# Kernel optimization log

Hardware: AMD Instinct MI355X
Metric: run time of the kernel (lower is better)

The kernel has to match this reference:

```python
import jax, jax.numpy as jnp
import numpy as np
from jax import lax

B, T, E, H = 32, 512, 256, 512

def setup_inputs() -> dict:
    key = jax.random.key(0)
    ks = jax.random.split(key, 7)
    s = 1.0 / np.sqrt(H)  # PyTorch RNN init range
    u = lambda k, sh: jax.random.uniform(k, sh, jnp.float32, -s, s)
    return {
        "xs": jax.random.normal(ks[0], (B, T, E), jnp.float32),
        "w_ih0": u(ks[1], (2, H, E)),      # [dir, H, in]
        "w_hh0": u(ks[2], (2, H, H)),
        "b0":    u(ks[3], (2, 2, H)),      # [dir, (b_ih,b_hh), H]
        "w_ih1": u(ks[4], (2, H, 2 * H)),
        "w_hh1": u(ks[5], (2, H, H)),
        "b1":    u(ks[6], (2, 2, H)),
    }

def _rnn_dir(x_tbi, w_ih, w_hh, b_ih, b_hh, reverse):
    # Precompute the input GEMM for all timesteps: [T,B,H]
    pre = jnp.einsum('tbi,hi->tbh', x_tbi, w_ih) + b_ih + b_hh
    h0 = jnp.zeros((x_tbi.shape[1], w_hh.shape[0]), x_tbi.dtype)
    def step(h, p):
        h = jnp.tanh(p + h @ w_hh.T)
        return h, h
    _, hs = lax.scan(step, h0, pre, reverse=reverse)  # ys aligned with xs order
    hy = hs[0] if reverse else hs[-1]
    return hs, hy

def _layer(x_tbi, w_ih, w_hh, b):
    hf, hyf = _rnn_dir(x_tbi, w_ih[0], w_hh[0], b[0, 0], b[0, 1], False)
    hb, hyb = _rnn_dir(x_tbi, w_ih[1], w_hh[1], b[1, 0], b[1, 1], True)
    return jnp.concatenate([hf, hb], axis=-1), jnp.stack([hyf, hyb])

def reference(xs, w_ih0, w_hh0, b0, w_ih1, w_hh1, b1):
    x = jnp.transpose(xs, (1, 0, 2))          # batch_first -> [T,B,E]
    h1, hy0 = _layer(x, w_ih0, w_hh0, b0)     # [T,B,2H], [2,B,H]
    h2, hy1 = _layer(h1, w_ih1, w_hh1, b1)
    hs = jnp.transpose(h2, (1, 0, 2))         # [B,T,2H]
    hy = jnp.concatenate([hy0, hy1], axis=0)  # [4,B,H] layer-major like PyTorch
    # F.dropout with p=0.0 is identity
    return (hs, hy)
```

## Files before the change

kernel.cpp:

```cpp
#include <hip/hip_runtime.h>
#include <hip/hip_fp16.h>


#define T_ 512
#define B_ 32
#define E_ 256
#define H_ 512

using half8 = _Float16 __attribute__((ext_vector_type(8)));
using f32x4 = float __attribute__((ext_vector_type(4)));
typedef unsigned long long u64;
typedef unsigned int u32;

static constexpr size_t OFF_PRE   = 0;
static constexpr size_t OFF_XH1   = 32ull << 20;
static constexpr size_t OFF_X0H   = 64ull << 20;
static constexpr size_t OFF_W0H   = 72ull << 20;
static constexpr size_t OFF_W1H   = OFF_W0H + (512ull << 10);
static constexpr size_t OFF_WHH   = OFF_W1H + (2ull << 20);
static constexpr size_t OFF_BS    = OFF_WHH + (2ull << 20);
static constexpr size_t OFF_HX    = OFF_BS + (8ull << 10);
static constexpr size_t OFF_FLG   = OFF_HX + (512ull << 10);
static constexpr size_t OFF_CTL   = OFF_FLG + 512;
static constexpr size_t ZERO_SIZE = (512ull << 10) + 1024;

static constexpr size_t HX_LAYER_STRIDE = 2 * 2 * 32 * 256;
static constexpr size_t HX_DIR_STRIDE   = 2 * 32 * 256;

__device__ __forceinline__ float fast_tanh(float x) {
    float cx = fminf(fmaxf(x, -9.0f), 9.0f);
    float e2 = __expf(2.0f * cx);
    return (e2 - 1.0f) * __builtin_amdgcn_rcpf(e2 + 1.0f);
}

__global__ void prep_kernel(const float* __restrict__ xs,
                            const float* __restrict__ wih0,
                            const float* __restrict__ whh0,
                            const float* __restrict__ b0,
                            const float* __restrict__ wih1,
                            const float* __restrict__ whh1,
                            const float* __restrict__ b1,
                            _Float16* __restrict__ x0h,
                            _Float16* __restrict__ w0h,
                            _Float16* __restrict__ w1h,
                            _Float16* __restrict__ whh,
                            float* __restrict__ bsum)
{
    const int N0 = T_ * B_ * E_;
    const int N1 = 2 * H_ * E_;
    const int N2 = 2 * H_ * 2*H_;
    const int N3 = 2 * H_ * H_;
    const int total = N0 + N1 + N2 + 2 * N3 + 2048;
    for (int idx = blockIdx.x * blockDim.x + threadIdx.x; idx < total;
         idx += gridDim.x * blockDim.x) {
        int i = idx;
        if (i < N0) {
            int t = i >> 13;
            int r = i & 8191;
            int b = r >> 8;
            int e = r & 255;
            x0h[i] = (_Float16)xs[((size_t)(b << 9) + t) * 256 + e];
        } else if ((i -= N0) < N1) {
            w0h[i] = (_Float16)wih0[i];
        } else if ((i -= N1) < N2) {
            w1h[i] = (_Float16)wih1[i];
        } else if ((i -= N2) < N3) {
            whh[i] = (_Float16)whh0[i];
        } else if ((i -= N3) < N3) {
            whh[N3 + i] = (_Float16)whh1[i];
        } else {
            i -= N3;
            int layer = i >> 10;
            int r = i & 1023;
            int d = r >> 9;
            int j = r & 511;
            const float* bb = layer ? b1 : b0;
            bsum[i] = bb[d * 1024 + j] + bb[d * 1024 + 512 + j];
        }
    }
}

__global__ __launch_bounds__(256, 2)
void gemm_kernel(const _Float16* __restrict__ X,
                 const _Float16* __restrict__ W,
                 const float* __restrict__ bias,
                 _Float16* __restrict__ out, int K)
{
    __shared__ _Float16 Ash[64][72];
    __shared__ _Float16 Bsh[64][72];
    const int m0 = blockIdx.x * 64, n0 = blockIdx.y * 64, d = blockIdx.z;
    const _Float16* Wd = W + (size_t)d * 512 * K;
    const int tid = threadIdx.x;
    const int l = tid & 63, w = tid >> 6;
    const int wm = w & 1, wn = w >> 1;
    const int lm = l & 15, q = l >> 4;
    f32x4 c[2][2] = {};
    for (int kk = 0; kk < K; kk += 64) {
        for (int ci = tid; ci < 512; ci += 256) {
            int row = ci >> 3, col = (ci & 7) * 8;
            *(half8*)&Ash[row][col] =
                *(const half8*)&X[(size_t)(m0 + row) * K + kk + col];
            *(half8*)&Bsh[row][col] =
                *(const half8*)&Wd[(size_t)(n0 + row) * K + kk + col];
        }
        __syncthreads();
        for (int kt = 0; kt < 2; ++kt) {
            const int kof = kt * 32 + q * 8;
            half8 a0 = *(const half8*)&Ash[wm * 32 + lm][kof];
            half8 a1 = *(const half8*)&Ash[wm * 32 + 16 + lm][kof];
            half8 b0f = *(const half8*)&Bsh[wn * 32 + lm][kof];
            half8 b1f = *(const half8*)&Bsh[wn * 32 + 16 + lm][kof];
            c[0][0] = __builtin_amdgcn_mfma_f32_16x16x32_f16(a0, b0f, c[0][0], 0, 0, 0);
            c[0][1] = __builtin_amdgcn_mfma_f32_16x16x32_f16(a0, b1f, c[0][1], 0, 0, 0);
            c[1][0] = __builtin_amdgcn_mfma_f32_16x16x32_f16(a1, b0f, c[1][0], 0, 0, 0);
            c[1][1] = __builtin_amdgcn_mfma_f32_16x16x32_f16(a1, b1f, c[1][1], 0, 0, 0);
        }
        __syncthreads();
    }
    _Float16* outd = out + (size_t)d * 16384 * 512;
    for (int mi = 0; mi < 2; ++mi)
        for (int ni = 0; ni < 2; ++ni) {
            int col = n0 + wn * 32 + ni * 16 + lm;
            float bv = bias[d * 512 + col];
            for (int r = 0; r < 4; ++r) {
                int rowm = m0 + wm * 32 + mi * 16 + q * 4 + r;
                outd[(size_t)rowm * 512 + col] = (_Float16)(c[mi][ni][r] + bv);
            }
        }
}

__global__ __launch_bounds__(256)
void rnn_kernel(const _Float16* __restrict__ pre,
                const _Float16* __restrict__ whh,
                u64* __restrict__ hx,
                u32* __restrict__ flgL,
                u32* __restrict__ ctl,
                _Float16* __restrict__ xh1,
                float* __restrict__ dout,
                int layer)
{
    __shared__ uint4 As[2][64 * 33];
    __shared__ int sh_role, sh_slot;

    const int tid = threadIdx.x;

    if (tid == 0) {
        int xcc;
        asm volatile("s_getreg_b32 %0, hwreg(HW_REG_XCC_ID)" : "=s"(xcc));
        xcc &= 7;
        u32 slot = __hip_atomic_fetch_add(&ctl[xcc], 1u, __ATOMIC_RELAXED,
                                          __HIP_MEMORY_SCOPE_SYSTEM);
        int role = 0;
        if (slot < 16u) {
            if (slot == 15u) {
                u32 r = __hip_atomic_fetch_add(&ctl[8], 1u, __ATOMIC_ACQ_REL,
                                               __HIP_MEMORY_SCOPE_SYSTEM);
                role = (r < 2u) ? (int)r + 1 : 3;
                __hip_atomic_store(&ctl[16 + xcc], (u32)role, __ATOMIC_RELEASE,
                                   __HIP_MEMORY_SCOPE_SYSTEM);
            } else {
                long it = 0;
                while (true) {
                    u32 r = __hip_atomic_load(&ctl[16 + xcc], __ATOMIC_ACQUIRE,
                                              __HIP_MEMORY_SCOPE_SYSTEM);
                    if (r) { role = (int)r; break; }
                    if (++it > 10000000) { role = 3; break; }
                }
            }
        }
        sh_role = role;
        sh_slot = (int)slot;
    }
    __syncthreads();
    const int role = sh_role;
    const int g = sh_slot;
    if (role == 0 || role == 3) return;
    const int d = role - 1;

    const int wv = tid >> 6, l = tid & 63;
    const int lm = l & 15, q = l >> 4;
    const int wm = wv & 1, wn = wv >> 1;
    const int jn = g * 32 + wn * 16;
    const int bA = wm * 16 + lm;
    const int bq = wm * 16 + q * 4;

    half8 Bf[16];
    {
        const _Float16* wrow = whh + ((size_t)d * 512 + jn + lm) * 512;
#pragma unroll
        for (int kt = 0; kt < 16; ++kt)
            Bf[kt] = *(const half8*)&wrow[kt * 32 + q * 8];
    }

    u64* hbd = hx + (size_t)d * HX_DIR_STRIDE;
    u32* flg = flgL + d * 32;
    const int jp_pub = (jn + (lm & ~1)) >> 1;
    const int scat_base = ((tid >> 2) * 33) * 4 + (tid & 3);

    for (int s = 0; s < T_; ++s) {
        const int t = d ? (T_ - 1 - s) : s;

        const _Float16* prow = pre + ((size_t)d * 16384 + (size_t)t * B_) * 512 + jn + lm;
        _Float16 pv[4];
#pragma unroll
        for (int r = 0; r < 4; ++r)
            pv[r] = prow[(size_t)(bq + r) * 512];

        {
            const u32 need = (u32)s;
            bool ok;
            do {
                u32 f = (l < 16)
                    ? __hip_atomic_load(&flg[l], __ATOMIC_RELAXED,
                                        __HIP_MEMORY_SCOPE_AGENT)
                    : 0xFFFFFFFFu;
                ok = __all(f >= need);
            } while (!ok);
        }

        const u64* src = hbd + (size_t)(s & 1) * 8192 + tid;
        const unsigned tag = (unsigned)s;
        u64 wvv[32];
        bool stale = true;
        do {
#pragma unroll
            for (int i = 0; i < 32; ++i)
                wvv[i] = __hip_atomic_load(&src[i * 256],
                                           __ATOMIC_RELAXED, __HIP_MEMORY_SCOPE_AGENT);
            bool ok = true;
#pragma unroll
            for (int i = 0; i < 32; ++i)
                ok &= ((unsigned)(wvv[i] >> 32) == tag);
            stale = __any(!ok);
        } while (stale);

        u32* AsW = (u32*)&As[s & 1][0];
#pragma unroll
        for (int i = 0; i < 32; ++i)
            AsW[scat_base + i * 4] = (u32)wvv[i];
        __syncthreads();

        f32x4 c0, c1;
#pragma unroll
        for (int r = 0; r < 4; ++r) { c0[r] = (float)pv[r]; c1[r] = 0.0f; }
#pragma unroll
        for (int kt = 0; kt < 16; ++kt) {
            union { uint4 u; half8 h; } cv;
            cv.u = As[s & 1][(kt * 4 + q) * 33 + bA];
            if (kt & 1) c1 = __builtin_amdgcn_mfma_f32_16x16x32_f16(cv.h, Bf[kt], c1, 0, 0, 0);
            else        c0 = __builtin_amdgcn_mfma_f32_16x16x32_f16(cv.h, Bf[kt], c0, 0, 0, 0);
        }

        u64* dst = hbd + (size_t)((s + 1) & 1) * 8192;
        const u64 tagw = ((u64)(unsigned)(s + 1)) << 32;
        const int j = jn + lm;
        float hv[4];
        unsigned hb[4];
#pragma unroll
        for (int r = 0; r < 4; ++r) {
            hv[r] = fast_tanh(c0[r] + c1[r]);
            union { _Float16 f; unsigned short u; } cb;
            cb.f = (_Float16)hv[r];
            hb[r] = cb.u;
        }
#pragma unroll
        for (int r = 0; r < 4; ++r) {
            unsigned p = __shfl_xor(hb[r], 1, 64);
            unsigned lo = (l & 1) ? p : hb[r];
            unsigned hi = (l & 1) ? hb[r] : p;
            if ((r >> 1) == (l & 1)) {
                u64 word = tagw | ((u64)hi << 16) | lo;
                __hip_atomic_store(&dst[(size_t)(bq + r) * 256 + jp_pub], word,
                                   __ATOMIC_RELAXED, __HIP_MEMORY_SCOPE_AGENT);
            }
        }
        __syncthreads();
        if (tid == 0)
            __hip_atomic_store(&flg[g], (u32)(s + 1), __ATOMIC_RELAXED,
                               __HIP_MEMORY_SCOPE_AGENT);

#pragma unroll
        for (int r = 0; r < 4; ++r) {
            const int b = bq + r;
            if (layer == 0) {
                xh1[((size_t)t * B_ + b) * 1024 + d * 512 + j] = (_Float16)hv[r];
            } else {
                dout[((size_t)b * T_ + t) * 1024 + d * 512 + j] = hv[r];
            }
            if (s == T_ - 1) {
                dout[16777216ull + ((size_t)(layer * 2 + d) * B_ + b) * 512 + j] = hv[r];
            }
        }
    }
}

extern "C" void kernel_launch(void* const* d_in, const int* in_sizes, int n_in,
                              void* d_out, int out_size, void* d_ws, size_t ws_size,
                              hipStream_t stream)
{
    const float* xs   = (const float*)d_in[0];
    const float* wih0 = (const float*)d_in[1];
    const float* whh0 = (const float*)d_in[2];
    const float* b0   = (const float*)d_in[3];
    const float* wih1 = (const float*)d_in[4];
    const float* whh1 = (const float*)d_in[5];
    const float* b1   = (const float*)d_in[6];

    char* ws = (char*)d_ws;
    _Float16* pre  = (_Float16*)(ws + OFF_PRE);
    _Float16* xh1  = (_Float16*)(ws + OFF_XH1);
    _Float16* x0h  = (_Float16*)(ws + OFF_X0H);
    _Float16* w0h  = (_Float16*)(ws + OFF_W0H);
    _Float16* w1h  = (_Float16*)(ws + OFF_W1H);
    _Float16* whh  = (_Float16*)(ws + OFF_WHH);
    float*    bsum = (float*)(ws + OFF_BS);
    u64*      hx   = (u64*)(ws + OFF_HX);
    u32*      flg  = (u32*)(ws + OFF_FLG);
    u32*      ctl  = (u32*)(ws + OFF_CTL);
    float*    out  = (float*)d_out;

    (void)hipMemsetAsync(ws + OFF_HX, 0, ZERO_SIZE, stream);

    prep_kernel<<<2048, 256, 0, stream>>>(xs, wih0, whh0, b0, wih1, whh1, b1,
                                          x0h, w0h, w1h, whh, bsum);

    gemm_kernel<<<dim3(256, 8, 2), 256, 0, stream>>>(x0h, w0h, bsum, pre, 256);
    rnn_kernel<<<256, 256, 0, stream>>>(pre, whh, hx, flg, ctl, xh1, out, 0);

    gemm_kernel<<<dim3(256, 8, 2), 256, 0, stream>>>(xh1, w1h, bsum + 1024, pre, 1024);
    rnn_kernel<<<256, 256, 0, stream>>>(pre, whh + 2 * 512 * 512,
                                        hx + HX_LAYER_STRIDE, flg + 64, ctl + 32,
                                        xh1, out, 1);
}
```

Measured before the change: 3.133 ms.

## Drop flag polling, batch hidden-state stores via LDS, spin idle blocks

```diff
diff --git a/kernel.cpp b/kernel.cpp
--- a/kernel.cpp
+++ b/kernel.cpp
@@ -20,8 +20,7 @@
 static constexpr size_t OFF_WHH   = OFF_W1H + (2ull << 20);
 static constexpr size_t OFF_BS    = OFF_WHH + (2ull << 20);
 static constexpr size_t OFF_HX    = OFF_BS + (8ull << 10);
-static constexpr size_t OFF_FLG   = OFF_HX + (512ull << 10);
-static constexpr size_t OFF_CTL   = OFF_FLG + 512;
+static constexpr size_t OFF_CTL   = OFF_HX + (512ull << 10);
 static constexpr size_t ZERO_SIZE = (512ull << 10) + 1024;
 
 static constexpr size_t HX_LAYER_STRIDE = 2 * 2 * 32 * 256;
@@ -31,6 +30,12 @@
     float cx = fminf(fmaxf(x, -9.0f), 9.0f);
     float e2 = __expf(2.0f * cx);
     return (e2 - 1.0f) * __builtin_amdgcn_rcpf(e2 + 1.0f);
+}
+
+__device__ __forceinline__ void lds_barrier() {
+    __builtin_amdgcn_sched_barrier(0);
+    asm volatile("s_waitcnt lgkmcnt(0)\n\ts_barrier" ::: "memory");
+    __builtin_amdgcn_sched_barrier(0);
 }
 
 __global__ void prep_kernel(const float* __restrict__ xs,
@@ -133,13 +138,13 @@
 void rnn_kernel(const _Float16* __restrict__ pre,
                 const _Float16* __restrict__ whh,
                 u64* __restrict__ hx,
-                u32* __restrict__ flgL,
                 u32* __restrict__ ctl,
                 _Float16* __restrict__ xh1,
                 float* __restrict__ dout,
                 int layer)
 {
     __shared__ uint4 As[2][64 * 33];
+    __shared__ float stF[8 * 32 * 36];
     __shared__ int sh_role, sh_slot;
 
     const int tid = threadIdx.x;
@@ -164,7 +169,7 @@
                     u32 r = __hip_atomic_load(&ctl[16 + xcc], __ATOMIC_ACQUIRE,
                                               __HIP_MEMORY_SCOPE_SYSTEM);
                     if (r) { role = (int)r; break; }
-                    if (++it > 10000000) { role = 3; break; }
+                    if (++it > 100000000) { role = 3; break; }
                 }
             }
         }
@@ -174,7 +179,23 @@
     __syncthreads();
     const int role = sh_role;
     const int g = sh_slot;
-    if (role == 0 || role == 3) return;
+    if (role == 0 || role == 3) {
+        float ha = 1.0f + (float)(tid & 31) * 1e-7f;
+        float hc = 1.0f - (float)(tid & 7) * 1e-7f;
+        for (int it = 0; it < 60000; ++it) {
+#pragma unroll 32
+            for (int u = 0; u < 32; ++u) {
+                ha = __builtin_fmaf(ha, 0.99999988f, 1e-9f);
+                hc = __builtin_fmaf(hc, 1.00000012f, -1e-9f);
+            }
+            if ((it & 15) == 0) {
+                if (__hip_atomic_load(&ctl[24], __ATOMIC_RELAXED,
+                                      __HIP_MEMORY_SCOPE_SYSTEM)) break;
+            }
+        }
+        asm volatile("" :: "v"(ha), "v"(hc));
+        return;
+    }
     const int d = role - 1;
 
     const int wv = tid >> 6, l = tid & 63;
@@ -183,6 +204,7 @@
     const int jn = g * 32 + wn * 16;
     const int bA = wm * 16 + lm;
     const int bq = wm * 16 + q * 4;
+    const int jl = wn * 16 + lm;
 
     half8 Bf[16];
     {
@@ -193,7 +215,6 @@
     }
 
     u64* hbd = hx + (size_t)d * HX_DIR_STRIDE;
-    u32* flg = flgL + d * 32;
     const int jp_pub = (jn + (lm & ~1)) >> 1;
     const int scat_base = ((tid >> 2) * 33) * 4 + (tid & 3);
 
@@ -205,40 +226,31 @@
 #pragma unroll
         for (int r = 0; r < 4; ++r)
             pv[r] = prow[(size_t)(bq + r) * 512];
-
-        {
-            const u32 need = (u32)s;
-            bool ok;
-            do {
-                u32 f = (l < 16)
-                    ? __hip_atomic_load(&flg[l], __ATOMIC_RELAXED,
-                                        __HIP_MEMORY_SCOPE_AGENT)
-                    : 0xFFFFFFFFu;
-                ok = __all(f >= need);
-            } while (!ok);
-        }
 
         const u64* src = hbd + (size_t)(s & 1) * 8192 + tid;
         const unsigned tag = (unsigned)s;
         u64 wvv[32];
-        bool stale = true;
-        do {
-#pragma unroll
-            for (int i = 0; i < 32; ++i)
-                wvv[i] = __hip_atomic_load(&src[i * 256],
-                                           __ATOMIC_RELAXED, __HIP_MEMORY_SCOPE_AGENT);
-            bool ok = true;
-#pragma unroll
-            for (int i = 0; i < 32; ++i)
-                ok &= ((unsigned)(wvv[i] >> 32) == tag);
-            stale = __any(!ok);
-        } while (stale);
+        {
+            bool stale = true;
+            long it = 0;
+            do {
+#pragma unroll
+                for (int i = 0; i < 32; ++i)
+                    wvv[i] = __hip_atomic_load(&src[i * 256],
+                                               __ATOMIC_RELAXED, __HIP_MEMORY_SCOPE_AGENT);
+                bool ok = true;
+#pragma unroll
+                for (int i = 0; i < 32; ++i)
+                    ok &= ((unsigned)(wvv[i] >> 32) == tag);
+                stale = __any(!ok);
+            } while (stale && ++it < 2000000);
+        }
 
         u32* AsW = (u32*)&As[s & 1][0];
 #pragma unroll
         for (int i = 0; i < 32; ++i)
             AsW[scat_base + i * 4] = (u32)wvv[i];
-        __syncthreads();
+        lds_barrier();
 
         f32x4 c0, c1;
 #pragma unroll
@@ -274,24 +286,43 @@
                                    __ATOMIC_RELAXED, __HIP_MEMORY_SCOPE_AGENT);
             }
         }
-        __syncthreads();
-        if (tid == 0)
-            __hip_atomic_store(&flg[g], (u32)(s + 1), __ATOMIC_RELAXED,
-                               __HIP_MEMORY_SCOPE_AGENT);
-
-#pragma unroll
-        for (int r = 0; r < 4; ++r) {
-            const int b = bq + r;
+
+#pragma unroll
+        for (int r = 0; r < 4; ++r)
+            stF[((s & 7) * 32 + (bq + r)) * 36 + jl] = hv[r];
+        if (s == T_ - 1) {
+#pragma unroll
+            for (int r = 0; r < 4; ++r)
+                dout[16777216ull + ((size_t)(layer * 2 + d) * B_ + (bq + r)) * 512 + j] = hv[r];
+        }
+
+        if ((s & 7) == 7) {
+            lds_barrier();
+            const int sp = tid >> 5, b = tid & 31;
+            const int ss = (s & ~7) | sp;
+            const int tt = d ? (T_ - 1 - ss) : ss;
+            const float* sf = &stF[(sp * 32 + b) * 36];
             if (layer == 0) {
-                xh1[((size_t)t * B_ + b) * 1024 + d * 512 + j] = (_Float16)hv[r];
+                _Float16* dp = xh1 + ((size_t)tt * B_ + b) * 1024 + d * 512 + g * 32;
+#pragma unroll
+                for (int k = 0; k < 4; ++k) {
+                    half8 h;
+#pragma unroll
+                    for (int e = 0; e < 8; ++e) h[e] = (_Float16)sf[k * 8 + e];
+                    *(half8*)&dp[k * 8] = h;
+                }
             } else {
-                dout[((size_t)b * T_ + t) * 1024 + d * 512 + j] = hv[r];
-            }
-            if (s == T_ - 1) {
-                dout[16777216ull + ((size_t)(layer * 2 + d) * B_ + b) * 512 + j] = hv[r];
-            }
-        }
-    }
+                float* dp = dout + ((size_t)b * T_ + tt) * 1024 + d * 512 + g * 32;
+#pragma unroll
+                for (int k = 0; k < 8; ++k)
+                    *(f32x4*)&dp[k * 4] = *(const f32x4*)&sf[k * 4];
+            }
+        }
+    }
+
+    if (tid == 0)
+        __hip_atomic_store(&ctl[24], 1u, __ATOMIC_RELAXED,
+                           __HIP_MEMORY_SCOPE_SYSTEM);
 }
 
 extern "C" void kernel_launch(void* const* d_in, const int* in_sizes, int n_in,
@@ -315,7 +346,6 @@
     _Float16* whh  = (_Float16*)(ws + OFF_WHH);
     float*    bsum = (float*)(ws + OFF_BS);
     u64*      hx   = (u64*)(ws + OFF_HX);
-    u32*      flg  = (u32*)(ws + OFF_FLG);
     u32*      ctl  = (u32*)(ws + OFF_CTL);
     float*    out  = (float*)d_out;
 
@@ -325,10 +355,10 @@
                                           x0h, w0h, w1h, whh, bsum);
 
     gemm_kernel<<<dim3(256, 8, 2), 256, 0, stream>>>(x0h, w0h, bsum, pre, 256);
-    rnn_kernel<<<256, 256, 0, stream>>>(pre, whh, hx, flg, ctl, xh1, out, 0);
+    rnn_kernel<<<256, 256, 0, stream>>>(pre, whh, hx, ctl, xh1, out, 0);
 
     gemm_kernel<<<dim3(256, 8, 2), 256, 0, stream>>>(xh1, w1h, bsum + 1024, pre, 1024);
     rnn_kernel<<<256, 256, 0, stream>>>(pre, whh + 2 * 512 * 512,
-                                        hx + HX_LAYER_STRIDE, flg + 64, ctl + 32,
+                                        hx + HX_LAYER_STRIDE, ctl + 32,
                                         xh1, out, 1);
 }
```

Measured after the change: 3.564 ms. 13.8% more time.
